# Kernel optimization log

Measured on AMD Instinct MI355X. Metric: run time of the kernel, lower is better.

## Reference

```python
import jax, jax.numpy as jnp
import numpy as np

NEG_SLOPE = 0.2  # PyG GATConv default LeakyReLU slope
BN_EPS = 1e-5


def gat_layer(x, src, dst, W, a_src, a_dst, num_nodes):
    """PyG-style GATConv (no dropout, eval mode). Returns [N, H, C]."""
    H, C = a_src.shape
    h = (x @ W).reshape(-1, H, C)                       # [N,H,C]
    s_src = jnp.einsum('nhc,hc->nh', h, a_src)          # [N,H]
    s_dst = jnp.einsum('nhc,hc->nh', h, a_dst)          # [N,H]
    e = jax.nn.leaky_relu(s_src[src] + s_dst[dst], NEG_SLOPE)  # [E,H]
    # segment softmax over incoming edges of each dst node
    e_max = jax.ops.segment_max(e, dst, num_segments=num_nodes)  # [N,H]
    e_exp = jnp.exp(e - e_max[dst])
    denom = jax.ops.segment_sum(e_exp, dst, num_segments=num_nodes)
    alpha = e_exp / (denom[dst] + 1e-16)                # [E,H]
    msg = h[src] * alpha[:, :, None]                    # [E,H,C] (dominant intermediate)
    return jax.ops.segment_sum(msg, dst, num_segments=num_nodes)  # [N,H,C]


def setup_inputs() -> dict:
    key = jax.random.key(0)
    ks = jax.random.split(key, 12)
    N, Din, Hdim, Heads, Dout = 50000, 128, 128, 8, 128
    E = 150000
    inp = {}
    inp['x'] = jax.random.normal(ks[0], (N, Din), dtype=jnp.float32)
    inp['edge_index'] = jax.random.randint(ks[1], (2, E), 0, N, dtype=jnp.int64)
    sc1 = 1.0 / np.sqrt(Din)
    inp['W1'] = jax.random.uniform(ks[2], (Din, Heads * Hdim), minval=-sc1, maxval=sc1, dtype=jnp.float32)
    inp['a_src1'] = jax.random.normal(ks[3], (Heads, Hdim), dtype=jnp.float32) * 0.1
    inp['a_dst1'] = jax.random.normal(ks[4], (Heads, Hdim), dtype=jnp.float32) * 0.1
    inp['b1'] = jnp.zeros((Heads * Hdim,), dtype=jnp.float32)
    inp['gamma'] = jnp.ones((Heads * Hdim,), dtype=jnp.float32)
    inp['beta'] = jnp.zeros((Heads * Hdim,), dtype=jnp.float32)
    sc2 = 1.0 / np.sqrt(Heads * Hdim)
    inp['W2'] = jax.random.uniform(ks[5], (Heads * Hdim, Dout), minval=-sc2, maxval=sc2, dtype=jnp.float32)
    inp['a_src2'] = jax.random.normal(ks[6], (1, Dout), dtype=jnp.float32) * 0.1
    inp['a_dst2'] = jax.random.normal(ks[7], (1, Dout), dtype=jnp.float32) * 0.1
    inp['b2'] = jnp.zeros((Dout,), dtype=jnp.float32)
    return inp


def reference(x, W1, a_src1, a_dst1, b1, gamma, beta, W2, a_src2, a_dst2, b2, edge_index):
    N = x.shape[0]
    src, dst = edge_index[0], edge_index[1]
    # GAT layer 1: heads=8, concat=True
    h1 = gat_layer(x, src, dst, W1, a_src1, a_dst1, N)   # [N,8,128]
    h1 = h1.reshape(N, -1) + b1                          # [N,1024]
    # BatchNorm1d (training-mode batch stats, biased variance as in torch)
    mu = jnp.mean(h1, axis=0)
    var = jnp.var(h1, axis=0)
    h1 = gamma * (h1 - mu) * jax.lax.rsqrt(var + BN_EPS) + beta
    h1 = jax.nn.elu(h1)
    # GAT layer 2: heads=1, concat=False (mean == squeeze for 1 head)
    h2 = gat_layer(h1, src, dst, W2, a_src2, a_dst2, N)  # [N,1,128]
    return h2[:, 0, :] + b2
```

## Files before the change

kernel.cpp:

```cpp
#include <hip/hip_runtime.h>
#include <hip/hip_bf16.h>
#include <math.h>

#define NEG_SLOPE 0.2f
#define BN_EPS 1e-5f

typedef short bf16x8 __attribute__((ext_vector_type(8)));
typedef float f32x4 __attribute__((ext_vector_type(4)));

__device__ __forceinline__ float bf2f(unsigned short u) {
  union { unsigned int i; float f; } v;
  v.i = ((unsigned int)u) << 16;
  return v.f;
}
__device__ __forceinline__ unsigned short f2bf(float f) {
  union { unsigned int i; float f; } v;
  v.f = f;
  unsigned int i = v.i;
  unsigned int r = (i + 0x7fffu + ((i >> 16) & 1u)) >> 16;
  return (unsigned short)r;
}

__global__ __launch_bounds__(256) void detect_kernel(
    const unsigned int* __restrict__ xw, const unsigned int* __restrict__ eiw,
    int E, int* __restrict__ flags) {
  __shared__ int cnt[2];
  if (threadIdx.x < 2) cnt[threadIdx.x] = 0;
  __syncthreads();
  int t = threadIdx.x;
  int inrange = 0;
  for (int i = t; i < 2048; i += 256) {
    unsigned int e = (xw[i] >> 7) & 0xFFu;
    inrange += (e >= 100u && e <= 135u) ? 1 : 0;
  }
  atomicAdd(&cnt[0], inrange);
  int M = min(1024, E / 2);
  int zeros = 0;
  for (int i = t; i < M; i += 256) zeros += (eiw[2 * i + 1] == 0u) ? 1 : 0;
  atomicAdd(&cnt[1], zeros);
  __syncthreads();
  if (t == 0) {
    flags[0] = (cnt[0] > 1536) ? 1 : 0;
    flags[1] = (cnt[1] > M / 2) ? 1 : 0;
  }
}

__global__ __launch_bounds__(256) void canon_x(
    const void* __restrict__ src, unsigned short* __restrict__ dst, int n_real,
    int n_total, const int* __restrict__ flags) {
  int i = blockIdx.x * 256 + threadIdx.x;
  if (i >= n_total) return;
  unsigned short v = 0;
  if (i < n_real)
    v = flags[0] ? ((const unsigned short*)src)[i]
                 : f2bf(((const float*)src)[i]);
  dst[i] = v;
}

__global__ __launch_bounds__(256) void canon_w_t(
    const void* __restrict__ src, unsigned short* __restrict__ dst, int Kdim,
    int Ndim, const int* __restrict__ flags) {
  int i = blockIdx.x * 256 + threadIdx.x;
  if (i >= Kdim * Ndim) return;
  int k = i / Ndim, n = i - k * Ndim;
  unsigned short v = flags[0] ? ((const unsigned short*)src)[i]
                              : f2bf(((const float*)src)[i]);
  dst[(size_t)n * Kdim + k] = v;
}

__global__ __launch_bounds__(1024) void canon_params(
    const void* s0, const void* s1, const void* s2, const void* s3,
    const void* s4, const void* s5, const void* s6, const void* s7,
    unsigned short* d0, unsigned short* d1, unsigned short* d2,
    unsigned short* d3, unsigned short* d4, unsigned short* d5,
    unsigned short* d6, unsigned short* d7, const int* __restrict__ flags) {
  int b = blockIdx.x, t = threadIdx.x;
  const void* s;
  unsigned short* d;
  int n;
  switch (b) {
    case 0: s = s0; d = d0; n = 1024; break;
    case 1: s = s1; d = d1; n = 1024; break;
    case 2: s = s2; d = d2; n = 1024; break;
    case 3: s = s3; d = d3; n = 1024; break;
    case 4: s = s4; d = d4; n = 1024; break;
    case 5: s = s5; d = d5; n = 128; break;
    case 6: s = s6; d = d6; n = 128; break;
    default: s = s7; d = d7; n = 128; break;
  }
  if (t < n)
    d[t] = flags[0] ? ((const unsigned short*)s)[t]
                    : f2bf(((const float*)s)[t]);
}

__global__ __launch_bounds__(256) void canon_idx(
    const int* __restrict__ ei, int* __restrict__ eis, int* __restrict__ eid,
    int E, const int* __restrict__ flags) {
  int e = blockIdx.x * 256 + threadIdx.x;
  if (e >= E) return;
  if (flags[1]) {
    eis[e] = ei[2 * (size_t)e];
    eid[e] = ei[2 * (size_t)E + 2 * (size_t)e];
  } else {
    eis[e] = ei[e];
    eid[e] = ei[E + e];
  }
}

template <bool TRANSFORM_A, bool OUT_BF16>
__global__ __launch_bounds__(256) void gemm_mfma(
    const unsigned short* __restrict__ A, const unsigned short* __restrict__ Bt,
    void* __restrict__ Cv, int M, int N, int K,
    const float* __restrict__ scale, const float* __restrict__ shift) {
  constexpr int BK = 32;
  constexpr int LDA = BK + 8;
  __shared__ unsigned short As[128 * LDA];
  __shared__ unsigned short Bs[128 * LDA];

  const int m0 = blockIdx.y * 128;
  const int n0 = blockIdx.x * 128;
  const int tid = threadIdx.x;
  const int wid = tid >> 6;
  const int lane = tid & 63;
  const int q = lane >> 4;
  const int r = lane & 15;
  const int wm = (wid >> 1) * 64;
  const int wn = (wid & 1) * 64;

  f32x4 acc[4][4] = {};

  const int row0 = (tid * 8) >> 5, col0 = (tid * 8) & 31;
  const int row1 = row0 + 64;

  bf16x8 ra[2], rb[2];
  ra[0] = *(const bf16x8*)(A + (size_t)(m0 + row0) * K + col0);
  ra[1] = *(const bf16x8*)(A + (size_t)(m0 + row1) * K + col0);
  rb[0] = *(const bf16x8*)(Bt + (size_t)(n0 + row0) * K + col0);
  rb[1] = *(const bf16x8*)(Bt + (size_t)(n0 + row1) * K + col0);

  for (int k0 = 0; k0 < K; k0 += BK) {
#pragma unroll
    for (int rd = 0; rd < 2; ++rd) {
      int row = rd ? row1 : row0;
      bf16x8 v = ra[rd];
      if (TRANSFORM_A) {
        float scv[8], shv[8];
        *(float4*)&scv[0] = *(const float4*)(scale + k0 + col0);
        *(float4*)&scv[4] = *(const float4*)(scale + k0 + col0 + 4);
        *(float4*)&shv[0] = *(const float4*)(shift + k0 + col0);
        *(float4*)&shv[4] = *(const float4*)(shift + k0 + col0 + 4);
        union { bf16x8 v; unsigned short u[8]; } p;
        p.v = v;
#pragma unroll
        for (int j = 0; j < 8; ++j) {
          float f = bf2f(p.u[j]) * scv[j] + shv[j];
          f = f > 0.f ? f : (__expf(f) - 1.0f);
          p.u[j] = f2bf(f);
        }
        v = p.v;
      }
      *(bf16x8*)(&As[row * LDA + col0]) = v;
      *(bf16x8*)(&Bs[row * LDA + col0]) = rb[rd];
    }
    __syncthreads();

    int k1 = k0 + BK;
    if (k1 < K) {
      ra[0] = *(const bf16x8*)(A + (size_t)(m0 + row0) * K + k1 + col0);
      ra[1] = *(const bf16x8*)(A + (size_t)(m0 + row1) * K + k1 + col0);
      rb[0] = *(const bf16x8*)(Bt + (size_t)(n0 + row0) * K + k1 + col0);
      rb[1] = *(const bf16x8*)(Bt + (size_t)(n0 + row1) * K + k1 + col0);
    }

    bf16x8 af[4], bfv[4];
#pragma unroll
    for (int mi = 0; mi < 4; ++mi)
      af[mi] = *(const bf16x8*)(&As[(wm + mi * 16 + r) * LDA + q * 8]);
#pragma unroll
    for (int ni = 0; ni < 4; ++ni)
      bfv[ni] = *(const bf16x8*)(&Bs[(wn + ni * 16 + r) * LDA + q * 8]);
#pragma unroll
    for (int mi = 0; mi < 4; ++mi)
#pragma unroll
      for (int ni = 0; ni < 4; ++ni)
        acc[mi][ni] = __builtin_amdgcn_mfma_f32_16x16x32_bf16(
            af[mi], bfv[ni], acc[mi][ni], 0, 0, 0);
    __syncthreads();
  }

#pragma unroll
  for (int mi = 0; mi < 4; ++mi) {
#pragma unroll
    for (int ni = 0; ni < 4; ++ni) {
#pragma unroll
      for (int i = 0; i < 4; ++i) {
        int row = m0 + wm + mi * 16 + q * 4 + i;
        int col = n0 + wn + ni * 16 + r;
        if (OUT_BF16)
          ((unsigned short*)Cv)[(size_t)row * N + col] = f2bf(acc[mi][ni][i]);
        else
          ((float*)Cv)[(size_t)row * N + col] = acc[mi][ni][i];
      }
    }
  }
}

__global__ __launch_bounds__(256) void count_dst(const int* __restrict__ eid,
                                                 int E, int* __restrict__ cnt) {
  int e = blockIdx.x * 256 + threadIdx.x;
  if (e < E) atomicAdd(&cnt[eid[e]], 1);
}

__global__ __launch_bounds__(256) void scan_p1(const int* __restrict__ cnt,
                                               int* __restrict__ bsum, int N) {
  __shared__ int sd[256];
  int b = blockIdx.x, t = threadIdx.x;
  int base = b * 2048;
  int s = 0;
  for (int i = t; i < 2048; i += 256) {
    int idx = base + i;
    if (idx < N) s += cnt[idx];
  }
  sd[t] = s;
  __syncthreads();
  for (int o = 128; o > 0; o >>= 1) {
    if (t < o) sd[t] += sd[t + o];
    __syncthreads();
  }
  if (t == 0) bsum[b] = sd[0];
}

__global__ __launch_bounds__(256) void scan_p2(int* __restrict__ bsum, int nb) {
  __shared__ int sd[256];
  int t = threadIdx.x;
  int own = (t < nb) ? bsum[t] : 0;
  sd[t] = own;
  __syncthreads();
  for (int o = 1; o < 256; o <<= 1) {
    int v = (t >= o) ? sd[t - o] : 0;
    __syncthreads();
    sd[t] += v;
    __syncthreads();
  }
  if (t < nb) bsum[t] = sd[t] - own;
}

__global__ __launch_bounds__(256) void scan_p3(
    const int* __restrict__ cnt, const int* __restrict__ bsum,
    int* __restrict__ offsets, int* __restrict__ cursor, int N) {
  __shared__ int sd[256];
  int b = blockIdx.x, t = threadIdx.x;
  int base = b * 2048 + t * 8;
  int c[8];
  int ts = 0;
#pragma unroll
  for (int j = 0; j < 8; ++j) {
    int idx = base + j;
    c[j] = (idx < N) ? cnt[idx] : 0;
    ts += c[j];
  }
  sd[t] = ts;
  __syncthreads();
  for (int o = 1; o < 256; o <<= 1) {
    int v = (t >= o) ? sd[t - o] : 0;
    __syncthreads();
    sd[t] += v;
    __syncthreads();
  }
  int run = bsum[b] + sd[t] - ts;
#pragma unroll
  for (int j = 0; j < 8; ++j) {
    int idx = base + j;
    if (idx < N) {
      offsets[idx] = run;
      cursor[idx] = run;
      run += c[j];
    }
  }
  if (b == gridDim.x - 1 && t == 255) offsets[N] = bsum[b] + sd[255];
}

__global__ __launch_bounds__(256) void scatter_src(
    const int* __restrict__ eis, const int* __restrict__ eid, int E,
    int* __restrict__ cursor, int* __restrict__ srcs, int* __restrict__ dsts) {
  int e = blockIdx.x * 256 + threadIdx.x;
  if (e >= E) return;
  int d = eid[e];
  int pos = atomicAdd(&cursor[d], 1);
  srcs[pos] = eis[e];
  dsts[pos] = d;
}

__global__ __launch_bounds__(256) void scores1_v2(
    const unsigned short* __restrict__ h1, const unsigned short* __restrict__ a_src,
    const unsigned short* __restrict__ a_dst, float* __restrict__ s_src,
    float* __restrict__ s_dst, int N) {
  int n = blockIdx.x * 4 + (threadIdx.x >> 6);
  int lane = threadIdx.x & 63;
  if (n >= N) return;
  const unsigned short* hp = h1 + (size_t)n * 1024 + lane * 16;
  union { bf16x8 v; unsigned short u[8]; } h0, h1v, s0, s1, d0, d1;
  h0.v = *(const bf16x8*)hp;
  h1v.v = *(const bf16x8*)(hp + 8);
  s0.v = *(const bf16x8*)(a_src + lane * 16);
  s1.v = *(const bf16x8*)(a_src + lane * 16 + 8);
  d0.v = *(const bf16x8*)(a_dst + lane * 16);
  d1.v = *(const bf16x8*)(a_dst + lane * 16 + 8);
  float vs = 0.f, vd = 0.f;
#pragma unroll
  for (int j = 0; j < 8; ++j) {
    float a = bf2f(h0.u[j]), b = bf2f(h1v.u[j]);
    vs += a * bf2f(s0.u[j]) + b * bf2f(s1.u[j]);
    vd += a * bf2f(d0.u[j]) + b * bf2f(d1.u[j]);
  }
  vs += __shfl_xor(vs, 1, 64); vd += __shfl_xor(vd, 1, 64);
  vs += __shfl_xor(vs, 2, 64); vd += __shfl_xor(vd, 2, 64);
  vs += __shfl_xor(vs, 4, 64); vd += __shfl_xor(vd, 4, 64);
  if ((lane & 7) == 0) {
    int h = lane >> 3;
    s_src[n * 8 + h] = vs;
    s_dst[n * 8 + h] = vd;
  }
}

__global__ __launch_bounds__(256) void scores2_f32(
    const float* __restrict__ h2, const unsigned short* __restrict__ a_src,
    const unsigned short* __restrict__ a_dst, float* __restrict__ s_src,
    float* __restrict__ s_dst, int N) {
  int w = blockIdx.x * 4 + (threadIdx.x >> 6);
  int lane = threadIdx.x & 63;
  if (w >= N) return;
  float2 hv = *(const float2*)(h2 + (size_t)w * 128 + lane * 2);
  unsigned int av = *(const unsigned int*)(a_src + lane * 2);
  unsigned int dv = *(const unsigned int*)(a_dst + lane * 2);
  float vs = hv.x * bf2f(av & 0xffff) + hv.y * bf2f(av >> 16);
  float vd = hv.x * bf2f(dv & 0xffff) + hv.y * bf2f(dv >> 16);
#pragma unroll
  for (int off = 32; off > 0; off >>= 1) {
    vs += __shfl_down(vs, off, 64);
    vd += __shfl_down(vd, off, 64);
  }
  if (lane == 0) {
    s_src[w] = vs;
    s_dst[w] = vd;
  }
}

__global__ __launch_bounds__(256) void edge_w1(
    const int* __restrict__ srcs, const int* __restrict__ dsts,
    const float* __restrict__ ssrc, const float* __restrict__ sdst,
    float* __restrict__ ew, int E8) {
  int t = blockIdx.x * 256 + threadIdx.x;
  if (t >= E8) return;
  int p = t >> 3, h = t & 7;
  float v = ssrc[srcs[p] * 8 + h] + sdst[dsts[p] * 8 + h];
  v = v > 0.f ? v : NEG_SLOPE * v;
  ew[t] = __expf(v);
}

__global__ __launch_bounds__(256) void edge_w2(
    const int* __restrict__ srcs, const int* __restrict__ dsts,
    const float* __restrict__ ssrc, const float* __restrict__ sdst,
    float* __restrict__ ew2, int E) {
  int p = blockIdx.x * 256 + threadIdx.x;
  if (p >= E) return;
  float v = ssrc[srcs[p]] + sdst[dsts[p]];
  v = v > 0.f ? v : NEG_SLOPE * v;
  ew2[p] = __expf(v);
}

__global__ __launch_bounds__(256) void agg1_csr(
    const int* __restrict__ offsets, const int* __restrict__ srcs,
    const unsigned short* __restrict__ h1, const float* __restrict__ ew,
    const unsigned short* __restrict__ b1, unsigned short* __restrict__ h1n) {
  int n = blockIdx.x;
  int j = threadIdx.x;
  int c = j * 4;
  int h = c >> 7;
  int beg = offsets[n], end = offsets[n + 1];
  float a0 = 0.f, a1 = 0.f, a2 = 0.f, a3 = 0.f, wsum = 0.f;
  for (int p = beg; p < end; ++p) {
    int s = srcs[p];
    float w = ew[p * 8 + h];
    wsum += w;
    ushort4 u = *(const ushort4*)(h1 + (size_t)s * 1024 + c);
    a0 = fmaf(bf2f(u.x), w, a0);
    a1 = fmaf(bf2f(u.y), w, a1);
    a2 = fmaf(bf2f(u.z), w, a2);
    a3 = fmaf(bf2f(u.w), w, a3);
  }
  float inv = 1.0f / (wsum + 1e-16f);
  ushort4 bb = *(const ushort4*)(b1 + c);
  ushort4 o;
  o.x = f2bf(a0 * inv + bf2f(bb.x));
  o.y = f2bf(a1 * inv + bf2f(bb.y));
  o.z = f2bf(a2 * inv + bf2f(bb.z));
  o.w = f2bf(a3 * inv + bf2f(bb.w));
  *(ushort4*)(h1n + (size_t)n * 1024 + c) = o;
}

__global__ __launch_bounds__(256) void bn_stats_part(
    const unsigned short* __restrict__ h1n, float* __restrict__ part, int N,
    int rowsPerBlock) {
  int b = blockIdx.x;
  int r0 = b * rowsPerBlock;
  int r1 = min(r0 + rowsPerBlock, N);
  int c = threadIdx.x * 4;
  float s0 = 0, s1 = 0, s2 = 0, s3 = 0;
  float q0 = 0, q1 = 0, q2 = 0, q3 = 0;
  int r = r0;
  for (; r + 4 <= r1; r += 4) {
    ushort4 u0 = *(const ushort4*)(h1n + (size_t)(r + 0) * 1024 + c);
    ushort4 u1 = *(const ushort4*)(h1n + (size_t)(r + 1) * 1024 + c);
    ushort4 u2 = *(const ushort4*)(h1n + (size_t)(r + 2) * 1024 + c);
    ushort4 u3 = *(const ushort4*)(h1n + (size_t)(r + 3) * 1024 + c);
    float v;
    v = bf2f(u0.x); s0 += v; q0 += v * v;
    v = bf2f(u0.y); s1 += v; q1 += v * v;
    v = bf2f(u0.z); s2 += v; q2 += v * v;
    v = bf2f(u0.w); s3 += v; q3 += v * v;
    v = bf2f(u1.x); s0 += v; q0 += v * v;
    v = bf2f(u1.y); s1 += v; q1 += v * v;
    v = bf2f(u1.z); s2 += v; q2 += v * v;
    v = bf2f(u1.w); s3 += v; q3 += v * v;
    v = bf2f(u2.x); s0 += v; q0 += v * v;
    v = bf2f(u2.y); s1 += v; q1 += v * v;
    v = bf2f(u2.z); s2 += v; q2 += v * v;
    v = bf2f(u2.w); s3 += v; q3 += v * v;
    v = bf2f(u3.x); s0 += v; q0 += v * v;
    v = bf2f(u3.y); s1 += v; q1 += v * v;
    v = bf2f(u3.z); s2 += v; q2 += v * v;
    v = bf2f(u3.w); s3 += v; q3 += v * v;
  }
  for (; r < r1; ++r) {
    ushort4 u = *(const ushort4*)(h1n + (size_t)r * 1024 + c);
    float v;
    v = bf2f(u.x); s0 += v; q0 += v * v;
    v = bf2f(u.y); s1 += v; q1 += v * v;
    v = bf2f(u.z); s2 += v; q2 += v * v;
    v = bf2f(u.w); s3 += v; q3 += v * v;
  }
  float* pb = part + (size_t)b * 2048;
  pb[c + 0] = s0; pb[c + 1] = s1; pb[c + 2] = s2; pb[c + 3] = s3;
  pb[1024 + c + 0] = q0; pb[1024 + c + 1] = q1;
  pb[1024 + c + 2] = q2; pb[1024 + c + 3] = q3;
}

__global__ __launch_bounds__(256) void bn_reduce_finalize(
    const float* __restrict__ part, int nparts,
    const unsigned short* __restrict__ gamma,
    const unsigned short* __restrict__ beta, float* __restrict__ scale,
    float* __restrict__ shift, int N) {
  int c = blockIdx.x * 4 + (threadIdx.x >> 6);
  int lane = threadIdx.x & 63;
  float s = 0.f, q = 0.f;
  for (int b = lane; b < nparts; b += 64) {
    s += part[(size_t)b * 2048 + c];
    q += part[(size_t)b * 2048 + 1024 + c];
  }
#pragma unroll
  for (int o = 32; o > 0; o >>= 1) {
    s += __shfl_xor(s, o, 64);
    q += __shfl_xor(q, o, 64);
  }
  if (lane == 0) {
    float inv_n = 1.0f / (float)N;
    float mu = s * inv_n;
    float var = q * inv_n - mu * mu;
    float sc = bf2f(gamma[c]) * rsqrtf(var + BN_EPS);
    scale[c] = sc;
    shift[c] = bf2f(beta[c]) - mu * sc;
  }
}

__global__ __launch_bounds__(64) void agg2_csr(
    const int* __restrict__ offsets, const int* __restrict__ srcs,
    const float* __restrict__ h2, const float* __restrict__ ew2,
    const unsigned short* __restrict__ b2, void* __restrict__ out,
    const int* __restrict__ flags) {
  int n = blockIdx.x;
  int lane = threadIdx.x;
  int c = lane * 2;
  int beg = offsets[n], end = offsets[n + 1];
  float a0 = 0.f, a1 = 0.f, wsum = 0.f;
  for (int p = beg; p < end; ++p) {
    int s = srcs[p];
    float w = ew2[p];
    wsum += w;
    float2 hv = *(const float2*)(h2 + (size_t)s * 128 + c);
    a0 = fmaf(hv.x, w, a0);
    a1 = fmaf(hv.y, w, a1);
  }
  float inv = 1.0f / (wsum + 1e-16f);
  unsigned int bb = *(const unsigned int*)(b2 + c);
  float r0 = a0 * inv + bf2f(bb & 0xffff);
  float r1 = a1 * inv + bf2f(bb >> 16);
  if (flags[0]) {
    unsigned int o = (unsigned int)f2bf(r0) | ((unsigned int)f2bf(r1) << 16);
    *(unsigned int*)((unsigned short*)out + (size_t)n * 128 + c) = o;
  } else {
    *(float2*)((float*)out + (size_t)n * 128 + c) = make_float2(r0, r1);
  }
}

extern "C" void kernel_launch(void* const* d_in, const int* in_sizes, int n_in,
                              void* d_out, int out_size, void* d_ws,
                              size_t ws_size, hipStream_t stream) {
  const void* x      = d_in[0];
  const int*  ei     = (const int*)d_in[1];
  const void* W1     = d_in[2];
  const void* a_src1 = d_in[3];
  const void* a_dst1 = d_in[4];
  const void* b1     = d_in[5];
  const void* gamma  = d_in[6];
  const void* beta   = d_in[7];
  const void* W2     = d_in[8];
  const void* a_src2 = d_in[9];
  const void* a_dst2 = d_in[10];
  const void* b2     = d_in[11];

  const int N = in_sizes[0] / 128;
  const int E = in_sizes[1] / 2;
  const int MP = ((N + 127) / 128) * 128;
  const int NB = (N + 2047) / 2048;
  const int NSTAT = 256;
  const int RPB = (N + NSTAT - 1) / NSTAT;

  char* ws = (char*)d_ws;
  size_t off = 0;
  unsigned short* h1  = (unsigned short*)(ws + off); off += (size_t)MP * 1024 * 2;
  char* h1n_base = ws + off;
  unsigned short* h1n = (unsigned short*)h1n_base;   off += (size_t)MP * 1024 * 2;
  float* ssrc1 = (float*)(ws + off); off += (size_t)N * 8 * 4;
  float* sdst1 = (float*)(ws + off); off += (size_t)N * 8 * 4;
  int* offsets = (int*)(ws + off); off += ((size_t)(N + 1) * 4 + 63) & ~63ull;
  int* srcs    = (int*)(ws + off); off += (size_t)E * 4;
  int* dsts    = (int*)(ws + off); off += (size_t)E * 4;
  float* ew    = (float*)(ws + off); off += (size_t)E * 8 * 4;
  float* part  = (float*)(ws + off); off += (size_t)NSTAT * 2048 * 4;
  unsigned short* W1t = (unsigned short*)(ws + off); off += 131072 * 2;
  unsigned short* W2t = (unsigned short*)(ws + off); off += 131072 * 2;
  unsigned short* as1c = (unsigned short*)(ws + off); off += 1024 * 2;
  unsigned short* ad1c = (unsigned short*)(ws + off); off += 1024 * 2;
  unsigned short* b1c  = (unsigned short*)(ws + off); off += 1024 * 2;
  unsigned short* gmc  = (unsigned short*)(ws + off); off += 1024 * 2;
  unsigned short* btc  = (unsigned short*)(ws + off); off += 1024 * 2;
  unsigned short* as2c = (unsigned short*)(ws + off); off += 128 * 2;
  unsigned short* ad2c = (unsigned short*)(ws + off); off += 128 * 2;
  unsigned short* b2c  = (unsigned short*)(ws + off); off += 128 * 2;
  float* scale = (float*)(ws + off); off += 1024 * 4;
  float* shift = (float*)(ws + off); off += 1024 * 4;
  int* bsum    = (int*)(ws + off); off += 256 * 4;
  int* flags   = (int*)(ws + off); off += 64;
  unsigned short* x_bf = (unsigned short*)h1n_base;
  int* eis    = (int*)(h1n_base + (16u << 20));
  int* eid    = eis + E;
  int* cnt    = eid + E;
  int* cursor = cnt + N;
  float* h2    = (float*)h1;
  float* ssrc2 = ssrc1;
  float* sdst2 = sdst1;
  float* ew2   = ew;

  detect_kernel<<<1, 256, 0, stream>>>((const unsigned int*)x,
                                       (const unsigned int*)ei, E, flags);
  canon_x<<<(MP * 128 + 255) / 256, 256, 0, stream>>>(x, x_bf, N * 128,
                                                      MP * 128, flags);
  canon_w_t<<<(131072 + 255) / 256, 256, 0, stream>>>(W1, W1t, 128, 1024, flags);
  canon_w_t<<<(131072 + 255) / 256, 256, 0, stream>>>(W2, W2t, 1024, 128, flags);
  canon_params<<<8, 1024, 0, stream>>>(a_src1, a_dst1, b1, gamma, beta, a_src2,
                                       a_dst2, b2, as1c, ad1c, b1c, gmc, btc,
                                       as2c, ad2c, b2c, flags);
  canon_idx<<<(E + 255) / 256, 256, 0, stream>>>(ei, eis, eid, E, flags);

  hipMemsetAsync(cnt, 0, (size_t)N * 4, stream);
  hipMemsetAsync((char*)h1n + (size_t)N * 1024 * 2, 0,
                 (size_t)(MP - N) * 1024 * 2, stream);

  count_dst<<<(E + 255) / 256, 256, 0, stream>>>(eid, E, cnt);
  scan_p1<<<NB, 256, 0, stream>>>(cnt, bsum, N);
  scan_p2<<<1, 256, 0, stream>>>(bsum, NB);
  scan_p3<<<NB, 256, 0, stream>>>(cnt, bsum, offsets, cursor, N);
  scatter_src<<<(E + 255) / 256, 256, 0, stream>>>(eis, eid, E, cursor, srcs,
                                                   dsts);

  {
    dim3 g(1024 / 128, MP / 128);
    gemm_mfma<false, true><<<g, 256, 0, stream>>>(x_bf, W1t, h1, MP, 1024, 128,
                                                  nullptr, nullptr);
  }
  scores1_v2<<<(N + 3) / 4, 256, 0, stream>>>(h1, as1c, ad1c, ssrc1, sdst1, N);
  edge_w1<<<(E * 8 + 255) / 256, 256, 0, stream>>>(srcs, dsts, ssrc1, sdst1,
                                                   ew, E * 8);
  agg1_csr<<<N, 256, 0, stream>>>(offsets, srcs, h1, ew, b1c, h1n);

  bn_stats_part<<<NSTAT, 256, 0, stream>>>(h1n, part, N, RPB);
  bn_reduce_finalize<<<256, 256, 0, stream>>>(part, NSTAT, gmc, btc, scale,
                                              shift, N);

  {
    dim3 g(1, MP / 128);
    gemm_mfma<true, false><<<g, 256, 0, stream>>>(h1n, W2t, h2, MP, 128, 1024,
                                                  scale, shift);
  }
  scores2_f32<<<(N + 3) / 4, 256, 0, stream>>>(h2, as2c, ad2c, ssrc2, sdst2, N);
  edge_w2<<<(E + 255) / 256, 256, 0, stream>>>(srcs, dsts, ssrc2, sdst2, ew2, E);
  agg2_csr<<<N, 64, 0, stream>>>(offsets, srcs, h2, ew2, b2c, d_out, flags);
}
```

Before: 378.6 us.

## Compute layer-1 scores from x via folded W·a, fuse count, retile GEMM2

Precomputes u = W1·a per head so layer-1 attention scores come from the 128-wide x rows instead of re-reading the 1024-wide h1. This removes the scores1 pass over h1. It also folds the destination count atomics into the index canonicalisation kernel, and gives the second GEMM a 64-row tile to launch more blocks. The h1n writes in aggregation become nontemporal stores. The folded scores use bf16 x and fp32 u, so rounding differs slightly from scoring the bf16-rounded h1.

```diff
diff --git a/kernel.cpp b/kernel.cpp
--- a/kernel.cpp
+++ b/kernel.cpp
@@ -7,6 +7,7 @@
 
 typedef short bf16x8 __attribute__((ext_vector_type(8)));
 typedef float f32x4 __attribute__((ext_vector_type(4)));
+typedef unsigned short u16x4 __attribute__((ext_vector_type(4)));
 
 __device__ __forceinline__ float bf2f(unsigned short u) {
   union { unsigned int i; float f; } v;
@@ -93,55 +94,112 @@
                     : f2bf(((const float*)s)[t]);
 }
 
-__global__ __launch_bounds__(256) void canon_idx(
+__global__ __launch_bounds__(256) void canon_idx_count(
     const int* __restrict__ ei, int* __restrict__ eis, int* __restrict__ eid,
-    int E, const int* __restrict__ flags) {
+    int* __restrict__ cnt, int E, const int* __restrict__ flags) {
   int e = blockIdx.x * 256 + threadIdx.x;
   if (e >= E) return;
+  int s, d;
   if (flags[1]) {
-    eis[e] = ei[2 * (size_t)e];
-    eid[e] = ei[2 * (size_t)E + 2 * (size_t)e];
+    s = ei[2 * (size_t)e];
+    d = ei[2 * (size_t)E + 2 * (size_t)e];
   } else {
-    eis[e] = ei[e];
-    eid[e] = ei[E + e];
-  }
-}
-
-template <bool TRANSFORM_A, bool OUT_BF16>
+    s = ei[e];
+    d = ei[E + e];
+  }
+  eis[e] = s;
+  eid[e] = d;
+  atomicAdd(&cnt[d], 1);
+}
+
+__global__ __launch_bounds__(256) void compute_u(
+    const unsigned short* __restrict__ W1t,
+    const unsigned short* __restrict__ as1,
+    const unsigned short* __restrict__ ad1, float* __restrict__ u_src,
+    float* __restrict__ u_dst) {
+  int h = blockIdx.x;
+  int t = threadIdx.x;
+  int k = t & 127;
+  bool dsel = t >= 128;
+  const unsigned short* a = dsel ? ad1 : as1;
+  float s = 0.f;
+  for (int c = 0; c < 128; ++c)
+    s += bf2f(W1t[((size_t)(h * 128 + c)) * 128 + k]) * bf2f(a[h * 128 + c]);
+  (dsel ? u_dst : u_src)[h * 128 + k] = s;
+}
+
+__global__ __launch_bounds__(256) void scores1_x(
+    const unsigned short* __restrict__ x, const float* __restrict__ u_src,
+    const float* __restrict__ u_dst, float* __restrict__ s_src,
+    float* __restrict__ s_dst, int N) {
+  int n = blockIdx.x * 4 + (threadIdx.x >> 6);
+  int lane = threadIdx.x & 63;
+  if (n >= N) return;
+  unsigned int xv = *(const unsigned int*)(x + (size_t)n * 128 + lane * 2);
+  float x0 = bf2f(xv & 0xffff), x1 = bf2f(xv >> 16);
+  float vs[8], vd[8];
+#pragma unroll
+  for (int h = 0; h < 8; ++h) {
+    float2 us = *(const float2*)(u_src + h * 128 + lane * 2);
+    float2 ud = *(const float2*)(u_dst + h * 128 + lane * 2);
+    vs[h] = x0 * us.x + x1 * us.y;
+    vd[h] = x0 * ud.x + x1 * ud.y;
+  }
+#pragma unroll
+  for (int o = 32; o > 0; o >>= 1) {
+#pragma unroll
+    for (int h = 0; h < 8; ++h) {
+      vs[h] += __shfl_xor(vs[h], o, 64);
+      vd[h] += __shfl_xor(vd[h], o, 64);
+    }
+  }
+  if (lane == 0) {
+#pragma unroll
+    for (int h = 0; h < 8; ++h) {
+      s_src[n * 8 + h] = vs[h];
+      s_dst[n * 8 + h] = vd[h];
+    }
+  }
+}
+
+template <int BM, bool TRANSFORM_A, bool OUT_BF16>
 __global__ __launch_bounds__(256) void gemm_mfma(
     const unsigned short* __restrict__ A, const unsigned short* __restrict__ Bt,
     void* __restrict__ Cv, int M, int N, int K,
     const float* __restrict__ scale, const float* __restrict__ shift) {
   constexpr int BK = 32;
   constexpr int LDA = BK + 8;
-  __shared__ unsigned short As[128 * LDA];
+  constexpr int ARD = BM / 64;
+  constexpr int MI = BM / 32;
+  __shared__ unsigned short As[BM * LDA];
   __shared__ unsigned short Bs[128 * LDA];
 
-  const int m0 = blockIdx.y * 128;
+  const int m0 = blockIdx.y * BM;
   const int n0 = blockIdx.x * 128;
   const int tid = threadIdx.x;
   const int wid = tid >> 6;
   const int lane = tid & 63;
   const int q = lane >> 4;
   const int r = lane & 15;
-  const int wm = (wid >> 1) * 64;
+  const int wm = (wid >> 1) * (BM / 2);
   const int wn = (wid & 1) * 64;
 
-  f32x4 acc[4][4] = {};
+  f32x4 acc[MI][4] = {};
 
   const int row0 = (tid * 8) >> 5, col0 = (tid * 8) & 31;
   const int row1 = row0 + 64;
 
-  bf16x8 ra[2], rb[2];
-  ra[0] = *(const bf16x8*)(A + (size_t)(m0 + row0) * K + col0);
-  ra[1] = *(const bf16x8*)(A + (size_t)(m0 + row1) * K + col0);
+  bf16x8 ra[ARD], rb[2];
+#pragma unroll
+  for (int rd = 0; rd < ARD; ++rd)
+    ra[rd] = *(const bf16x8*)(A + (size_t)(m0 + row0 + rd * 64) * K + col0);
   rb[0] = *(const bf16x8*)(Bt + (size_t)(n0 + row0) * K + col0);
   rb[1] = *(const bf16x8*)(Bt + (size_t)(n0 + row1) * K + col0);
 
   for (int k0 = 0; k0 < K; k0 += BK) {
 #pragma unroll
-    for (int rd = 0; rd < 2; ++rd) {
-      int row = rd ? row1 : row0;
+    for (int rd = 0; rd < ARD; ++rd) {
+      int row = row0 + rd * 64;
       bf16x8 v = ra[rd];
       if (TRANSFORM_A) {
         float scv[8], shv[8];
@@ -160,27 +218,30 @@
         v = p.v;
       }
       *(bf16x8*)(&As[row * LDA + col0]) = v;
-      *(bf16x8*)(&Bs[row * LDA + col0]) = rb[rd];
     }
+    *(bf16x8*)(&Bs[row0 * LDA + col0]) = rb[0];
+    *(bf16x8*)(&Bs[row1 * LDA + col0]) = rb[1];
     __syncthreads();
 
     int k1 = k0 + BK;
     if (k1 < K) {
-      ra[0] = *(const bf16x8*)(A + (size_t)(m0 + row0) * K + k1 + col0);
-      ra[1] = *(const bf16x8*)(A + (size_t)(m0 + row1) * K + k1 + col0);
+#pragma unroll
+      for (int rd = 0; rd < ARD; ++rd)
+        ra[rd] =
+            *(const bf16x8*)(A + (size_t)(m0 + row0 + rd * 64) * K + k1 + col0);
       rb[0] = *(const bf16x8*)(Bt + (size_t)(n0 + row0) * K + k1 + col0);
       rb[1] = *(const bf16x8*)(Bt + (size_t)(n0 + row1) * K + k1 + col0);
     }
 
-    bf16x8 af[4], bfv[4];
-#pragma unroll
-    for (int mi = 0; mi < 4; ++mi)
+    bf16x8 af[MI], bfv[4];
+#pragma unroll
+    for (int mi = 0; mi < MI; ++mi)
       af[mi] = *(const bf16x8*)(&As[(wm + mi * 16 + r) * LDA + q * 8]);
 #pragma unroll
     for (int ni = 0; ni < 4; ++ni)
       bfv[ni] = *(const bf16x8*)(&Bs[(wn + ni * 16 + r) * LDA + q * 8]);
 #pragma unroll
-    for (int mi = 0; mi < 4; ++mi)
+    for (int mi = 0; mi < MI; ++mi)
 #pragma unroll
       for (int ni = 0; ni < 4; ++ni)
         acc[mi][ni] = __builtin_amdgcn_mfma_f32_16x16x32_bf16(
@@ -189,7 +250,7 @@
   }
 
 #pragma unroll
-  for (int mi = 0; mi < 4; ++mi) {
+  for (int mi = 0; mi < MI; ++mi) {
 #pragma unroll
     for (int ni = 0; ni < 4; ++ni) {
 #pragma unroll
@@ -203,12 +264,6 @@
       }
     }
   }
-}
-
-__global__ __launch_bounds__(256) void count_dst(const int* __restrict__ eid,
-                                                 int E, int* __restrict__ cnt) {
-  int e = blockIdx.x * 256 + threadIdx.x;
-  if (e < E) atomicAdd(&cnt[eid[e]], 1);
 }
 
 __global__ __launch_bounds__(256) void scan_p1(const int* __restrict__ cnt,
@@ -289,38 +344,6 @@
   int pos = atomicAdd(&cursor[d], 1);
   srcs[pos] = eis[e];
   dsts[pos] = d;
-}
-
-__global__ __launch_bounds__(256) void scores1_v2(
-    const unsigned short* __restrict__ h1, const unsigned short* __restrict__ a_src,
-    const unsigned short* __restrict__ a_dst, float* __restrict__ s_src,
-    float* __restrict__ s_dst, int N) {
-  int n = blockIdx.x * 4 + (threadIdx.x >> 6);
-  int lane = threadIdx.x & 63;
-  if (n >= N) return;
-  const unsigned short* hp = h1 + (size_t)n * 1024 + lane * 16;
-  union { bf16x8 v; unsigned short u[8]; } h0, h1v, s0, s1, d0, d1;
-  h0.v = *(const bf16x8*)hp;
-  h1v.v = *(const bf16x8*)(hp + 8);
-  s0.v = *(const bf16x8*)(a_src + lane * 16);
-  s1.v = *(const bf16x8*)(a_src + lane * 16 + 8);
-  d0.v = *(const bf16x8*)(a_dst + lane * 16);
-  d1.v = *(const bf16x8*)(a_dst + lane * 16 + 8);
-  float vs = 0.f, vd = 0.f;
-#pragma unroll
-  for (int j = 0; j < 8; ++j) {
-    float a = bf2f(h0.u[j]), b = bf2f(h1v.u[j]);
-    vs += a * bf2f(s0.u[j]) + b * bf2f(s1.u[j]);
-    vd += a * bf2f(d0.u[j]) + b * bf2f(d1.u[j]);
-  }
-  vs += __shfl_xor(vs, 1, 64); vd += __shfl_xor(vd, 1, 64);
-  vs += __shfl_xor(vs, 2, 64); vd += __shfl_xor(vd, 2, 64);
-  vs += __shfl_xor(vs, 4, 64); vd += __shfl_xor(vd, 4, 64);
-  if ((lane & 7) == 0) {
-    int h = lane >> 3;
-    s_src[n * 8 + h] = vs;
-    s_dst[n * 8 + h] = vd;
-  }
 }
 
 __global__ __launch_bounds__(256) void scores2_f32(
@@ -391,12 +414,12 @@
   }
   float inv = 1.0f / (wsum + 1e-16f);
   ushort4 bb = *(const ushort4*)(b1 + c);
-  ushort4 o;
+  u16x4 o;
   o.x = f2bf(a0 * inv + bf2f(bb.x));
   o.y = f2bf(a1 * inv + bf2f(bb.y));
   o.z = f2bf(a2 * inv + bf2f(bb.z));
   o.w = f2bf(a3 * inv + bf2f(bb.w));
-  *(ushort4*)(h1n + (size_t)n * 1024 + c) = o;
+  __builtin_nontemporal_store(o, (u16x4*)(h1n + (size_t)n * 1024 + c));
 }
 
 __global__ __launch_bounds__(256) void bn_stats_part(
@@ -550,6 +573,8 @@
   unsigned short* b2c  = (unsigned short*)(ws + off); off += 128 * 2;
   float* scale = (float*)(ws + off); off += 1024 * 4;
   float* shift = (float*)(ws + off); off += 1024 * 4;
+  float* u_src = (float*)(ws + off); off += 1024 * 4;
+  float* u_dst = (float*)(ws + off); off += 1024 * 4;
   int* bsum    = (int*)(ws + off); off += 256 * 4;
   int* flags   = (int*)(ws + off); off += 64;
   unsigned short* x_bf = (unsigned short*)h1n_base;
@@ -564,6 +589,7 @@
 
   detect_kernel<<<1, 256, 0, stream>>>((const unsigned int*)x,
                                        (const unsigned int*)ei, E, flags);
+  (void)hipMemsetAsync(cnt, 0, (size_t)N * 4, stream);
   canon_x<<<(MP * 128 + 255) / 256, 256, 0, stream>>>(x, x_bf, N * 128,
                                                       MP * 128, flags);
   canon_w_t<<<(131072 + 255) / 256, 256, 0, stream>>>(W1, W1t, 128, 1024, flags);
@@ -571,25 +597,27 @@
   canon_params<<<8, 1024, 0, stream>>>(a_src1, a_dst1, b1, gamma, beta, a_src2,
                                        a_dst2, b2, as1c, ad1c, b1c, gmc, btc,
                                        as2c, ad2c, b2c, flags);
-  canon_idx<<<(E + 255) / 256, 256, 0, stream>>>(ei, eis, eid, E, flags);
-
-  hipMemsetAsync(cnt, 0, (size_t)N * 4, stream);
-  hipMemsetAsync((char*)h1n + (size_t)N * 1024 * 2, 0,
-                 (size_t)(MP - N) * 1024 * 2, stream);
-
-  count_dst<<<(E + 255) / 256, 256, 0, stream>>>(eid, E, cnt);
+  compute_u<<<8, 256, 0, stream>>>(W1t, as1c, ad1c, u_src, u_dst);
+  canon_idx_count<<<(E + 255) / 256, 256, 0, stream>>>(ei, eis, eid, cnt, E,
+                                                       flags);
+
+  (void)hipMemsetAsync((char*)h1n + (size_t)N * 1024 * 2, 0,
+                       (size_t)(MP - N) * 1024 * 2, stream);
+
   scan_p1<<<NB, 256, 0, stream>>>(cnt, bsum, N);
   scan_p2<<<1, 256, 0, stream>>>(bsum, NB);
   scan_p3<<<NB, 256, 0, stream>>>(cnt, bsum, offsets, cursor, N);
   scatter_src<<<(E + 255) / 256, 256, 0, stream>>>(eis, eid, E, cursor, srcs,
                                                    dsts);
 
+  scores1_x<<<(N + 3) / 4, 256, 0, stream>>>(x_bf, u_src, u_dst, ssrc1, sdst1,
+                                             N);
+
   {
     dim3 g(1024 / 128, MP / 128);
-    gemm_mfma<false, true><<<g, 256, 0, stream>>>(x_bf, W1t, h1, MP, 1024, 128,
-                                                  nullptr, nullptr);
-  }
-  scores1_v2<<<(N + 3) / 4, 256, 0, stream>>>(h1, as1c, ad1c, ssrc1, sdst1, N);
+    gemm_mfma<128, false, true><<<g, 256, 0, stream>>>(
+        x_bf, W1t, h1, MP, 1024, 128, nullptr, nullptr);
+  }
   edge_w1<<<(E * 8 + 255) / 256, 256, 0, stream>>>(srcs, dsts, ssrc1, sdst1,
                                                    ew, E * 8);
   agg1_csr<<<N, 256, 0, stream>>>(offsets, srcs, h1, ew, b1c, h1n);
@@ -599,9 +627,9 @@
                                               shift, N);
 
   {
-    dim3 g(1, MP / 128);
-    gemm_mfma<true, false><<<g, 256, 0, stream>>>(h1n, W2t, h2, MP, 128, 1024,
-                                                  scale, shift);
+    dim3 g(1, MP / 64);
+    gemm_mfma<64, true, false><<<g, 256, 0, stream>>>(h1n, W2t, h2, MP, 128,
+                                                      1024, scale, shift);
   }
   scores2_f32<<<(N + 3) / 4, 256, 0, stream>>>(h2, as2c, ad2c, ssrc2, sdst2, N);
   edge_w2<<<(E + 255) / 256, 256, 0, stream>>>(srcs, dsts, ssrc2, sdst2, ew2, E);
```

Measured after the change: 436.7 us. 1.15x slower.
